# Optimization experiments

Hardware: AMD Instinct MI355X
Metric: run time of the kernel (lower is better)

## Reference

```python
import jax, jax.numpy as jnp
import numpy as np

B, T, H, L, O = 256, 512, 512, 2, 2

def setup_inputs() -> dict:
    key = jax.random.key(0)
    ks = jax.random.split(key, 9)
    s = 0.05
    return {
        "x": jax.random.normal(ks[0], (B, T), jnp.float32),
        # input-side gate weights, layer 0 (input dim 1); gate order: [r, z, n]
        "Wi0": jax.random.normal(ks[1], (3, H, 1), jnp.float32) * s,
        "bi0": jax.random.normal(ks[2], (3, H), jnp.float32) * s,
        # input-side gate weights, layers 1..L-1 (input dim H)
        "Wi_rest": jax.random.normal(ks[3], (L - 1, 3, H, H), jnp.float32) * s,
        "bi_rest": jax.random.normal(ks[4], (L - 1, 3, H), jnp.float32) * s,
        # hidden-side gate weights for all layers
        "Wh": jax.random.normal(ks[5], (L, 3, H, H), jnp.float32) * s,
        "bh": jax.random.normal(ks[6], (L, 3, H), jnp.float32) * s,
        "fc_w": jax.random.normal(ks[7], (O, H), jnp.float32) * s,
        "fc_b": jax.random.normal(ks[8], (O,), jnp.float32) * s,
    }


def reference(x, Wi0, bi0, Wi_rest, bi_rest, Wh, bh, fc_w, fc_b):
    nL = Wh.shape[0]
    hsz = Wh.shape[-1]
    bsz = x.shape[0]

    def step(h, x_t):  # h: [L, B, H], x_t: [B]
        inp = x_t[:, None]  # [B, 1]
        new_h = []
        for l in range(nL):
            # fuse the 3 input-side and 3 hidden-side gate GEMMs into one einsum each
            if l == 0:
                gi = jnp.einsum('bi,ghi->gbh', inp, Wi0) + bi0[:, None, :]
            else:
                gi = jnp.einsum('bi,ghi->gbh', inp, Wi_rest[l - 1]) + bi_rest[l - 1, :, None, :]
            gh = jnp.einsum('bi,ghi->gbh', h[l], Wh[l]) + bh[l, :, None, :]
            r = jax.nn.sigmoid(gi[0] + gh[0])
            z = jax.nn.sigmoid(gi[1] + gh[1])
            n = jnp.tanh(gi[2] + r * gh[2])
            hl = (1.0 - z) * n + z * h[l]
            new_h.append(hl)
            inp = hl
        return jnp.stack(new_h), None

    h0 = jnp.zeros((nL, bsz, hsz), x.dtype)
    h_final, _ = jax.lax.scan(step, h0, x.T)  # scan over time axis
    return h_final[-1] @ fc_w.T + fc_b  # [B, O]
```

## Files before the change

### kernel.cpp

```cpp
#include <hip/hip_runtime.h>


#define TLEN 512
#define HDIM 512
#define MROW 16
#define NL0  8
#define NGRP 16
#define GRID 384
#define U0   64
#define U1   32
#define HSZE (MROW*HDIM)
#define ROWB 1040
#define DEPTH 4

#define RT_BAR 10000000ULL

typedef __attribute__((ext_vector_type(8))) short bf16x8;
typedef __attribute__((ext_vector_type(4))) float f32x4;

#define AT_LD64(p)   __hip_atomic_load((const unsigned long long*)(p), __ATOMIC_RELAXED, __HIP_MEMORY_SCOPE_AGENT)
#define AT_LD32(p)   __hip_atomic_load((const unsigned*)(p), __ATOMIC_RELAXED, __HIP_MEMORY_SCOPE_AGENT)
#define AT_ST16(p,v) __hip_atomic_store((unsigned short*)(p), (v), __ATOMIC_RELAXED, __HIP_MEMORY_SCOPE_AGENT)
#define AT_ST32(p,v) __hip_atomic_store((unsigned*)(p), (v), __ATOMIC_RELAXED, __HIP_MEMORY_SCOPE_AGENT)
#define AT_ST32F(p,v) __hip_atomic_store((float*)(p), (v), __ATOMIC_RELAXED, __HIP_MEMORY_SCOPE_AGENT)

__device__ __forceinline__ unsigned short f2bf(float f){
  unsigned u = __builtin_bit_cast(unsigned, f);
  u = (u + 0x7FFFu + ((u>>16)&1u)) >> 16;
  return (unsigned short)u;
}
__device__ __forceinline__ float sigm(float v){ return __builtin_amdgcn_rcpf(1.f + __expf(-v)); }
__device__ __forceinline__ float tanh_f(float v){ return 1.f - 2.f*__builtin_amdgcn_rcpf(__expf(2.f*v)+1.f); }

__device__ __forceinline__ bool wait_flags(unsigned* fl, int tA, int tB, int* sab){
  if (threadIdx.x < 64){
    const int lane = threadIdx.x;
    const int tgt = (lane<8) ? tA : (lane<24 ? tB : (int)0x80000000);
    const unsigned long long t0 = __builtin_amdgcn_s_memrealtime();
    int ab = 0;
    for(;;){
      int f = (lane<24) ? (int)AT_LD32(fl + lane*16) : 0x7fffffff;
      if (__ballot(f >= tgt) == ~0ULL) break;
      if (__builtin_amdgcn_s_memrealtime() - t0 > RT_BAR){ ab = 1; break; }
      __builtin_amdgcn_s_sleep(1);
    }
    if (lane==0) *sab = ab;
  }
  __syncthreads();
  __builtin_amdgcn_sched_barrier(0);
  return *sab != 0;
}

__device__ __forceinline__ void stage8(const unsigned short* src, unsigned short* shDst, int tid){
  unsigned long long hb[8];
  #pragma unroll
  for (int i=0;i<8;++i)
    hb[i] = AT_LD64((const char*)src + tid*8 + i*2048);
  #pragma unroll
  for (int i=0;i<8;++i){
    int flat = tid*8 + i*2048;
    *(unsigned long long*)((char*)shDst + (flat>>10)*ROWB + (flat&1023)) = hb[i];
  }
}

extern "C" __global__ void __launch_bounds__(256,2)
gru_persistent(const float* __restrict__ x,
               const float* __restrict__ Wi0,
               const float* __restrict__ bi0,
               const float* __restrict__ Wi1,
               const float* __restrict__ bi1,
               const float* __restrict__ Wh,
               const float* __restrict__ bh,
               const float* __restrict__ fcw,
               const float* __restrict__ fcb,
               float* __restrict__ out,
               unsigned* __restrict__ flg,
               unsigned short* __restrict__ h0g,
               unsigned short* __restrict__ h1g,
               float* __restrict__ h1f)
{
  __shared__ unsigned short shA[MROW*(ROWB/2)];
  __shared__ unsigned short shB[MROW*(ROWB/2)];
  __shared__ float shG[MROW*192];
  __shared__ int s_ab;

  const int tid  = threadIdx.x;
  const int lane = tid & 63;
  const int w    = tid >> 6;
  const int grp  = blockIdx.x & (NGRP-1);
  const int wgid = blockIdx.x >> 4;
  const int g16  = grp*MROW;

  unsigned* fl = flg + grp*512;
  unsigned short* h0 = h0g + grp*DEPTH*HSZE;
  unsigned short* h1 = h1g + grp*DEPTH*HSZE;

  if (grp & 1){
    const unsigned long long t0 = __builtin_amdgcn_s_memrealtime();
    while (__builtin_amdgcn_s_memrealtime() - t0 < 200ULL)
      __builtin_amdgcn_s_sleep(1);
  }

  if (wgid < NL0){
    const int u0   = wgid*U0;
    const int colb = w*48;

    bf16x8 bfr[3][16];
    #pragma unroll
    for (int nt=0; nt<3; ++nt){
      int col = colb + nt*16 + (lane&15);
      int g = col>>6, uu = col&63;
      const float* wrow = Wh + (size_t)(g*HDIM + u0 + uu)*HDIM;
      #pragma unroll
      for (int ks=0; ks<16; ++ks){
        int k = ks*32 + (lane>>4)*8;
        const float4 f0 = *(const float4*)(wrow + k);
        const float4 f1 = *(const float4*)(wrow + k + 4);
        bf16x8 v;
        v[0]=(short)f2bf(f0.x); v[1]=(short)f2bf(f0.y); v[2]=(short)f2bf(f0.z); v[3]=(short)f2bf(f0.w);
        v[4]=(short)f2bf(f1.x); v[5]=(short)f2bf(f1.y); v[6]=(short)f2bf(f1.z); v[7]=(short)f2bf(f1.w);
        bfr[nt][ks]=v;
      }
    }
    const int ua   = tid & 63;
    const int brow = (tid>>6)*4;
    float wi0v[3], bi0v[3], bh0v[3];
    #pragma unroll
    for (int g=0; g<3; ++g){
      wi0v[g] = Wi0[g*HDIM + u0+ua];
      bi0v[g] = bi0[g*HDIM + u0+ua];
      bh0v[g] = bh [g*HDIM + u0+ua];
    }
    float h_own[4];
    #pragma unroll
    for (int j=0;j<4;++j) h_own[j]=0.f;

    for (int s=0; s<TLEN; ++s){
      float xv[4];
      #pragma unroll
      for (int j=0;j<4;++j) xv[j] = x[(g16+brow+j)*TLEN + s];

      if (wait_flags(fl, s, s-3, &s_ab)) return;

      stage8(h0 + ((s-1)&3)*HSZE, shA, tid);
      __syncthreads();
      f32x4 acc[3] = {};
      #pragma unroll
      for (int ks=0; ks<16; ++ks){
        int koff = ks*64 + (lane>>4)*16;
        bf16x8 a0 = *(const bf16x8*)((const char*)shA + (lane&15)*ROWB + koff);
        #pragma unroll
        for (int nt=0; nt<3; ++nt)
          acc[nt] = __builtin_amdgcn_mfma_f32_16x16x32_bf16(a0, bfr[nt][ks], acc[nt],0,0,0);
      }
      #pragma unroll
      for (int nt=0; nt<3; ++nt)
        #pragma unroll
        for (int j=0;j<4;++j){
          int b = (lane>>4)*4 + j;
          shG[b*192 + colb + nt*16 + (lane&15)] = acc[nt][j];
        }
      __syncthreads();
      unsigned short* dstA = h0 + (s&3)*HSZE;
      #pragma unroll
      for (int j=0;j<4;++j){
        int b = brow + j;
        float G0 = shG[b*192 + ua]       + bh0v[0];
        float G1 = shG[b*192 + 64 + ua]  + bh0v[1];
        float G2 = shG[b*192 + 128 + ua] + bh0v[2];
        float r_ = sigm(fmaf(xv[j], wi0v[0], bi0v[0]) + G0);
        float z_ = sigm(fmaf(xv[j], wi0v[1], bi0v[1]) + G1);
        float n_ = tanh_f(fmaf(xv[j], wi0v[2], bi0v[2]) + r_*G2);
        float hn = (1.f - z_)*n_ + z_*h_own[j];
        h_own[j] = hn;
        AT_ST16(&dstA[b*HDIM + u0 + ua], f2bf(hn));
      }
      asm volatile("s_waitcnt vmcnt(0)" ::: "memory");
      __syncthreads();
      if (tid==0) AT_ST32(fl + wgid*16, (unsigned)(s+1));
    }
    if (wgid==0){
      if (wait_flags(fl, (int)0x80000000, TLEN, &s_ab)) return;
      if (tid < 128){
        int p = tid>>2, kl = tid&3;
        int b = p>>1, o = p&1;
        const char* h8 = (const char*)(h1f + (size_t)(g16+b)*HDIM + kl*128);
        const float2* w2 = (const float2*)(fcw + o*HDIM + kl*128);
        float a2 = 0.f;
        #pragma unroll
        for (int k=0;k<64;++k){
          unsigned long long v = AT_LD64(h8 + k*8);
          float2 hv = __builtin_bit_cast(float2, v);
          float2 wv = w2[k];
          a2 = fmaf(hv.x, wv.x, fmaf(hv.y, wv.y, a2));
        }
        a2 += __shfl_xor(a2, 1);
        a2 += __shfl_xor(a2, 2);
        if (kl==0) out[(g16+b)*2 + o] = a2 + fcb[o];
      }
    }
  } else {
    const int u1   = (wgid-NL0)*U1;
    const int colb = (w<2) ? w*48 : 96 + (w-2)*48;

    bf16x8 bfr[3][16];
    #pragma unroll
    for (int nt=0; nt<3; ++nt){
      int col = colb + nt*16 + (lane&15);
      const float* wrow;
      if (w < 2){ int g = col>>5, uu = col&31;
        wrow = Wi1 + (size_t)(g*HDIM + u1 + uu)*HDIM;
      } else {    int c2 = col-96; int g = c2>>5, uu = c2&31;
        wrow = Wh + (size_t)((3+g)*HDIM + u1 + uu)*HDIM;
      }
      #pragma unroll
      for (int ks=0; ks<16; ++ks){
        int k = ks*32 + (lane>>4)*8;
        const float4 f0 = *(const float4*)(wrow + k);
        const float4 f1 = *(const float4*)(wrow + k + 4);
        bf16x8 v;
        v[0]=(short)f2bf(f0.x); v[1]=(short)f2bf(f0.y); v[2]=(short)f2bf(f0.z); v[3]=(short)f2bf(f0.w);
        v[4]=(short)f2bf(f1.x); v[5]=(short)f2bf(f1.y); v[6]=(short)f2bf(f1.z); v[7]=(short)f2bf(f1.w);
        bfr[nt][ks]=v;
      }
    }
    const int ua   = tid & 31;
    const int brow = (tid>>5)*2;
    float bi1v[3], bh1v[3];
    #pragma unroll
    for (int g=0; g<3; ++g){
      bi1v[g] = bi1[g*HDIM + u1+ua];
      bh1v[g] = bh [(3+g)*HDIM + u1+ua];
    }
    float h_own[2];
    #pragma unroll
    for (int j=0;j<2;++j) h_own[j]=0.f;

    for (int t=1; t<=TLEN; ++t){
      const unsigned short* srcA = h0 + ((t-1)&3)*HSZE;
      const unsigned short* srcB = h1 + ((t-2)&3)*HSZE;

      if (wait_flags(fl, (int)0x80000000, t-1, &s_ab)) return;
      unsigned long long hb1[8];
      #pragma unroll
      for (int i=0;i<8;++i)
        hb1[i] = AT_LD64((const char*)srcB + tid*8 + i*2048);

      if (wait_flags(fl, t, (int)0x80000000, &s_ab)) return;
      unsigned long long hb0[8];
      #pragma unroll
      for (int i=0;i<8;++i)
        hb0[i] = AT_LD64((const char*)srcA + tid*8 + i*2048);

      #pragma unroll
      for (int i=0;i<8;++i){
        int flat = tid*8 + i*2048;
        *(unsigned long long*)((char*)shA + (flat>>10)*ROWB + (flat&1023)) = hb0[i];
        *(unsigned long long*)((char*)shB + (flat>>10)*ROWB + (flat&1023)) = hb1[i];
      }
      __syncthreads();
      const char* shSrc = (w<2) ? (const char*)shA : (const char*)shB;
      f32x4 acc[3] = {};
      #pragma unroll
      for (int ks=0; ks<16; ++ks){
        int koff = ks*64 + (lane>>4)*16;
        bf16x8 a0 = *(const bf16x8*)(shSrc + (lane&15)*ROWB + koff);
        #pragma unroll
        for (int nt=0; nt<3; ++nt)
          acc[nt] = __builtin_amdgcn_mfma_f32_16x16x32_bf16(a0, bfr[nt][ks], acc[nt],0,0,0);
      }
      #pragma unroll
      for (int nt=0; nt<3; ++nt)
        #pragma unroll
        for (int j=0;j<4;++j){
          int b = (lane>>4)*4 + j;
          shG[b*192 + colb + nt*16 + (lane&15)] = acc[nt][j];
        }
      __syncthreads();
      unsigned short* dstB = h1 + ((t-1)&3)*HSZE;
      #pragma unroll
      for (int j=0;j<2;++j){
        int b = brow + j;
        float gi0 = shG[b*192 + ua]        + bi1v[0];
        float gi1 = shG[b*192 + 32 + ua]   + bi1v[1];
        float gi2 = shG[b*192 + 64 + ua]   + bi1v[2];
        float gh0 = shG[b*192 + 96 + ua]   + bh1v[0];
        float gh1 = shG[b*192 + 128 + ua]  + bh1v[1];
        float gh2 = shG[b*192 + 160 + ua]  + bh1v[2];
        float r_ = sigm(gi0+gh0);
        float z_ = sigm(gi1+gh1);
        float n_ = tanh_f(gi2 + r_*gh2);
        float hn = (1.f - z_)*n_ + z_*h_own[j];
        h_own[j] = hn;
        AT_ST16(&dstB[b*HDIM + u1 + ua], f2bf(hn));
        if (t == TLEN) AT_ST32F(&h1f[(size_t)(g16+b)*HDIM + u1 + ua], hn);
      }
      asm volatile("s_waitcnt vmcnt(0)" ::: "memory");
      __syncthreads();
      if (tid==0) AT_ST32(fl + wgid*16, (unsigned)t);
    }
  }
}

extern "C" void kernel_launch(void* const* d_in, const int* in_sizes, int n_in,
                              void* d_out, int out_size, void* d_ws, size_t ws_size,
                              hipStream_t stream)
{
  const float* x   = (const float*)d_in[0];
  const float* Wi0 = (const float*)d_in[1];
  const float* bi0 = (const float*)d_in[2];
  const float* Wi1 = (const float*)d_in[3];
  const float* bi1 = (const float*)d_in[4];
  const float* Wh  = (const float*)d_in[5];
  const float* bh  = (const float*)d_in[6];
  const float* fcw = (const float*)d_in[7];
  const float* fcb = (const float*)d_in[8];
  float* out = (float*)d_out;

  unsigned*       flg = (unsigned*)d_ws;
  unsigned short* h0g = (unsigned short*)((char*)d_ws + 32768);
  unsigned short* h1g = (unsigned short*)((char*)d_ws + 32768 + 1048576);
  float*          h1f = (float*)((char*)d_ws + 32768 + 2*1048576);

  hipMemsetAsync(d_ws, 0, 32768 + 2*1048576 + 524288, stream);
  gru_persistent<<<GRID, 256, 0, stream>>>(x,Wi0,bi0,Wi1,bi1,Wh,bh,fcw,fcb,out,
                                           flg,h0g,h1g,h1f);
}
```

Before: 2.159 ms.

## Split batch into 32 groups of 8 rows with 768 persistent workgroups

```diff
diff --git a/kernel.cpp b/kernel.cpp
--- a/kernel.cpp
+++ b/kernel.cpp
@@ -3,10 +3,10 @@
 
 #define TLEN 512
 #define HDIM 512
-#define MROW 16
+#define MROW 8
 #define NL0  8
-#define NGRP 16
-#define GRID 384
+#define NGRP 32
+#define GRID 768
 #define U0   64
 #define U1   32
 #define HSZE (MROW*HDIM)
@@ -51,19 +51,27 @@
   return *sab != 0;
 }
 
-__device__ __forceinline__ void stage8(const unsigned short* src, unsigned short* shDst, int tid){
-  unsigned long long hb[8];
+__device__ __forceinline__ void stage4(const unsigned short* src, unsigned short* shDst, int tid){
+  unsigned long long hb[4];
   #pragma unroll
-  for (int i=0;i<8;++i)
+  for (int i=0;i<4;++i)
     hb[i] = AT_LD64((const char*)src + tid*8 + i*2048);
   #pragma unroll
-  for (int i=0;i<8;++i){
+  for (int i=0;i<4;++i){
     int flat = tid*8 + i*2048;
     *(unsigned long long*)((char*)shDst + (flat>>10)*ROWB + (flat&1023)) = hb[i];
   }
 }
 
-extern "C" __global__ void __launch_bounds__(256,2)
+__device__ __forceinline__ void zero_upper(unsigned short* shDst, int tid){
+  #pragma unroll
+  for (int i=0;i<4;++i){
+    int flat = tid*8 + i*2048;
+    *(unsigned long long*)((char*)shDst + (8 + (flat>>10))*ROWB + (flat&1023)) = 0ULL;
+  }
+}
+
+extern "C" __global__ void __launch_bounds__(256,3)
 gru_persistent(const float* __restrict__ x,
                const float* __restrict__ Wi0,
                const float* __restrict__ bi0,
@@ -79,25 +87,27 @@
                unsigned short* __restrict__ h1g,
                float* __restrict__ h1f)
 {
-  __shared__ unsigned short shA[MROW*(ROWB/2)];
-  __shared__ unsigned short shB[MROW*(ROWB/2)];
+  __shared__ unsigned short shA[16*(ROWB/2)];
+  __shared__ unsigned short shB[16*(ROWB/2)];
   __shared__ float shG[MROW*192];
   __shared__ int s_ab;
 
   const int tid  = threadIdx.x;
   const int lane = tid & 63;
   const int w    = tid >> 6;
-  const int grp  = blockIdx.x & (NGRP-1);
-  const int wgid = blockIdx.x >> 4;
-  const int g16  = grp*MROW;
+  const int bid  = blockIdx.x;
+  const int grp  = (bid + (bid>>8)) & (NGRP-1);
+  const int wgid = bid >> 5;
+  const int g8   = grp*MROW;
 
   unsigned* fl = flg + grp*512;
   unsigned short* h0 = h0g + grp*DEPTH*HSZE;
   unsigned short* h1 = h1g + grp*DEPTH*HSZE;
 
-  if (grp & 1){
+  if (grp % 3){
     const unsigned long long t0 = __builtin_amdgcn_s_memrealtime();
-    while (__builtin_amdgcn_s_memrealtime() - t0 < 200ULL)
+    const unsigned long long d  = (unsigned long long)(grp % 3) * 150ULL;
+    while (__builtin_amdgcn_s_memrealtime() - t0 < d)
       __builtin_amdgcn_s_sleep(1);
   }
 
@@ -123,7 +133,7 @@
       }
     }
     const int ua   = tid & 63;
-    const int brow = (tid>>6)*4;
+    const int brow = (tid>>6)*2;
     float wi0v[3], bi0v[3], bh0v[3];
     #pragma unroll
     for (int g=0; g<3; ++g){
@@ -131,18 +141,19 @@
       bi0v[g] = bi0[g*HDIM + u0+ua];
       bh0v[g] = bh [g*HDIM + u0+ua];
     }
-    float h_own[4];
-    #pragma unroll
-    for (int j=0;j<4;++j) h_own[j]=0.f;
+    float h_own[2];
+    h_own[0]=0.f; h_own[1]=0.f;
+
+    zero_upper(shA, tid);
 
     for (int s=0; s<TLEN; ++s){
-      float xv[4];
-      #pragma unroll
-      for (int j=0;j<4;++j) xv[j] = x[(g16+brow+j)*TLEN + s];
+      float xv[2];
+      #pragma unroll
+      for (int j=0;j<2;++j) xv[j] = x[(g8+brow+j)*TLEN + s];
 
       if (wait_flags(fl, s, s-3, &s_ab)) return;
 
-      stage8(h0 + ((s-1)&3)*HSZE, shA, tid);
+      stage4(h0 + ((s-1)&3)*HSZE, shA, tid);
       __syncthreads();
       f32x4 acc[3] = {};
       #pragma unroll
@@ -158,12 +169,12 @@
         #pragma unroll
         for (int j=0;j<4;++j){
           int b = (lane>>4)*4 + j;
-          shG[b*192 + colb + nt*16 + (lane&15)] = acc[nt][j];
+          if (b < MROW) shG[b*192 + colb + nt*16 + (lane&15)] = acc[nt][j];
         }
       __syncthreads();
       unsigned short* dstA = h0 + (s&3)*HSZE;
       #pragma unroll
-      for (int j=0;j<4;++j){
+      for (int j=0;j<2;++j){
         int b = brow + j;
         float G0 = shG[b*192 + ua]       + bh0v[0];
         float G1 = shG[b*192 + 64 + ua]  + bh0v[1];
@@ -181,10 +192,10 @@
     }
     if (wgid==0){
       if (wait_flags(fl, (int)0x80000000, TLEN, &s_ab)) return;
-      if (tid < 128){
+      if (tid < 64){
         int p = tid>>2, kl = tid&3;
         int b = p>>1, o = p&1;
-        const char* h8 = (const char*)(h1f + (size_t)(g16+b)*HDIM + kl*128);
+        const char* h8 = (const char*)(h1f + (size_t)(g8+b)*HDIM + kl*128);
         const float2* w2 = (const float2*)(fcw + o*HDIM + kl*128);
         float a2 = 0.f;
         #pragma unroll
@@ -196,7 +207,7 @@
         }
         a2 += __shfl_xor(a2, 1);
         a2 += __shfl_xor(a2, 2);
-        if (kl==0) out[(g16+b)*2 + o] = a2 + fcb[o];
+        if (kl==0) out[(g8+b)*2 + o] = a2 + fcb[o];
       }
     }
   } else {
@@ -225,35 +236,36 @@
       }
     }
     const int ua   = tid & 31;
-    const int brow = (tid>>5)*2;
+    const int brow = tid>>5;
     float bi1v[3], bh1v[3];
     #pragma unroll
     for (int g=0; g<3; ++g){
       bi1v[g] = bi1[g*HDIM + u1+ua];
       bh1v[g] = bh [(3+g)*HDIM + u1+ua];
     }
-    float h_own[2];
-    #pragma unroll
-    for (int j=0;j<2;++j) h_own[j]=0.f;
+    float h_own0 = 0.f;
+
+    zero_upper(shA, tid);
+    zero_upper(shB, tid);
 
     for (int t=1; t<=TLEN; ++t){
       const unsigned short* srcA = h0 + ((t-1)&3)*HSZE;
       const unsigned short* srcB = h1 + ((t-2)&3)*HSZE;
 
       if (wait_flags(fl, (int)0x80000000, t-1, &s_ab)) return;
-      unsigned long long hb1[8];
-      #pragma unroll
-      for (int i=0;i<8;++i)
+      unsigned long long hb1[4];
+      #pragma unroll
+      for (int i=0;i<4;++i)
         hb1[i] = AT_LD64((const char*)srcB + tid*8 + i*2048);
 
       if (wait_flags(fl, t, (int)0x80000000, &s_ab)) return;
-      unsigned long long hb0[8];
-      #pragma unroll
-      for (int i=0;i<8;++i)
+      unsigned long long hb0[4];
+      #pragma unroll
+      for (int i=0;i<4;++i)
         hb0[i] = AT_LD64((const char*)srcA + tid*8 + i*2048);
 
       #pragma unroll
-      for (int i=0;i<8;++i){
+      for (int i=0;i<4;++i){
         int flat = tid*8 + i*2048;
         *(unsigned long long*)((char*)shA + (flat>>10)*ROWB + (flat&1023)) = hb0[i];
         *(unsigned long long*)((char*)shB + (flat>>10)*ROWB + (flat&1023)) = hb1[i];
@@ -274,13 +286,12 @@
         #pragma unroll
         for (int j=0;j<4;++j){
           int b = (lane>>4)*4 + j;
-          shG[b*192 + colb + nt*16 + (lane&15)] = acc[nt][j];
+          if (b < MROW) shG[b*192 + colb + nt*16 + (lane&15)] = acc[nt][j];
         }
       __syncthreads();
       unsigned short* dstB = h1 + ((t-1)&3)*HSZE;
-      #pragma unroll
-      for (int j=0;j<2;++j){
-        int b = brow + j;
+      {
+        int b = brow;
         float gi0 = shG[b*192 + ua]        + bi1v[0];
         float gi1 = shG[b*192 + 32 + ua]   + bi1v[1];
         float gi2 = shG[b*192 + 64 + ua]   + bi1v[2];
@@ -290,10 +301,10 @@
         float r_ = sigm(gi0+gh0);
         float z_ = sigm(gi1+gh1);
         float n_ = tanh_f(gi2 + r_*gh2);
-        float hn = (1.f - z_)*n_ + z_*h_own[j];
-        h_own[j] = hn;
+        float hn = (1.f - z_)*n_ + z_*h_own0;
+        h_own0 = hn;
         AT_ST16(&dstB[b*HDIM + u1 + ua], f2bf(hn));
-        if (t == TLEN) AT_ST32F(&h1f[(size_t)(g16+b)*HDIM + u1 + ua], hn);
+        if (t == TLEN) AT_ST32F(&h1f[(size_t)(g8+b)*HDIM + u1 + ua], hn);
       }
       asm volatile("s_waitcnt vmcnt(0)" ::: "memory");
       __syncthreads();
@@ -318,11 +329,11 @@
   float* out = (float*)d_out;
 
   unsigned*       flg = (unsigned*)d_ws;
-  unsigned short* h0g = (unsigned short*)((char*)d_ws + 32768);
-  unsigned short* h1g = (unsigned short*)((char*)d_ws + 32768 + 1048576);
-  float*          h1f = (float*)((char*)d_ws + 32768 + 2*1048576);
-
-  hipMemsetAsync(d_ws, 0, 32768 + 2*1048576 + 524288, stream);
+  unsigned short* h0g = (unsigned short*)((char*)d_ws + 65536);
+  unsigned short* h1g = (unsigned short*)((char*)d_ws + 65536 + 1048576);
+  float*          h1f = (float*)((char*)d_ws + 65536 + 2*1048576);
+
+  hipMemsetAsync(d_ws, 0, 65536 + 2*1048576 + 524288, stream);
   gru_persistent<<<GRID, 256, 0, stream>>>(x,Wi0,bi0,Wi1,bi1,Wh,bh,fcw,fcb,out,
                                            flg,h0g,h1g,h1f);
 }
```

New measurement: 7.241 ms. 3.35x slower.
